# Performance work log

Hardware: AMD Instinct MI355X
Metric: run time of the kernel (lower is better)

## Reference

```python
import jax, jax.numpy as jnp
import numpy as np

S, B, DENC, DD, DE, V, T = 49, 64, 512, 1800, 512, 10000, 20


def setup_inputs() -> dict:
    key = jax.random.key(0)
    ks = jax.random.split(key, 16)
    g = lambda i, shape: jax.random.normal(ks[i], shape, jnp.float32) * 0.02
    z = lambda *shape: jnp.zeros(shape, jnp.float32)
    return {
        "h": jax.random.normal(ks[0], (S, B, DENC), jnp.float32),
        "E": jax.random.randint(ks[1], (T, B), 0, V),
        "emb": g(2, (V, DE)),
        "attn_W1": g(3, (DD, DD + DENC)), "attn_b1": z(DD),
        "attn_w2": g(4, (DD,)), "attn_b2": z(),
        "beta_w": g(5, (DD,)), "beta_b": z(),
        "W_ih": g(6, (4 * DD, DE + DENC)), "W_hh": g(7, (4 * DD, DD)),
        "b_ih": z(4 * DD), "b_hh": z(4 * DD),
        "out_W": g(8, (V, DD + DE + DENC)), "out_b": z(V),
        "ih_W1": g(9, (DD, DENC)), "ih_b1": z(DD), "ih_W2": g(10, (DD, DD)), "ih_b2": z(DD),
        "ic_W1": g(11, (DD, DENC)), "ic_b1": z(DD), "ic_W2": g(12, (DD, DD)), "ic_b2": z(DD),
    }


def _mlp(x, W1, b1, W2, b2):
    return jax.nn.relu(x @ W1.T + b1) @ W2.T + b2


def reference(h, E, emb, attn_W1, attn_b1, attn_w2, attn_b2, beta_w, beta_b,
              W_ih, W_hh, b_ih, b_hh, out_W, out_b,
              ih_W1, ih_b1, ih_W2, ih_b2, ic_W1, ic_b1, ic_W2, ic_b2):
    # h: (S, B, DENC) encoder annotations; E: (T, B) teacher tokens.
    h_avg = h.mean(axis=0)                        # (B, DENC)
    h0 = _mlp(h_avg, ih_W1, ih_b1, ih_W2, ih_b2)  # (B, DD)
    c0 = _mlp(h_avg, ic_W1, ic_b1, ic_W2, ic_b2)  # (B, DD)
    tok0 = jnp.zeros((h.shape[1],), jnp.int32)    # first y_tm1 is token 0

    def step(carry, e_t):
        ht, ct, prev_tok = carry
        # --- additive attention (queries=ht, keys=values=h) ---
        qexp = jnp.broadcast_to(ht[None], h.shape[:2] + (ht.shape[-1],))  # (S,B,DD)
        zpre = jnp.concatenate([qexp, h], axis=-1)                        # (S,B,DD+DENC)
        u = jax.nn.relu(zpre @ attn_W1.T + attn_b1) @ attn_w2 + attn_b2   # (S,B)
        a = jax.nn.softmax(u, axis=0)                                     # softmax over seq
        ctx = jnp.einsum('sb,sbe->be', a, h)                              # (B,DENC)
        beta = jax.nn.sigmoid(ht @ beta_w + beta_b)                       # (B,)
        ctx = ctx * beta[:, None]
        # --- LSTM cell on [embed(E_tm1); context] ---
        x = jnp.concatenate([emb[e_t], ctx], axis=-1)                     # (B,DE+DENC)
        gates = x @ W_ih.T + b_ih + ht @ W_hh.T + b_hh                    # (B,4*DD)
        i_g, f_g, g_g, o_g = jnp.split(gates, 4, axis=-1)
        c_new = jax.nn.sigmoid(f_g) * ct + jax.nn.sigmoid(i_g) * jnp.tanh(g_g)
        h_new = jax.nn.sigmoid(o_g) * jnp.tanh(c_new)
        # --- deep output layer: [h_t; embed(argmax prev logits); ctx] ---
        y_emb = emb[prev_tok]
        logits = jnp.concatenate([h_new, y_emb, ctx], axis=-1) @ out_W.T + out_b
        return (h_new, c_new, jnp.argmax(logits, axis=-1).astype(jnp.int32)), logits

    _, logits = jax.lax.scan(step, (h0, c0, tok0), E[:-1])
    return logits  # (T-1, B, V)
```

## Files before the change

### kernel.cpp

```cpp
#include <hip/hip_runtime.h>
#include <hip/hip_bf16.h>
#include <cmath>


namespace {

constexpr int S = 49, B = 64, DENC = 512, DD = 1800, DE = 512, V = 10000, T = 20;
constexpr int KC = DD + DE + DENC;
constexpr int G4 = 4 * DD;
constexpr int KCP = 2848;
constexpr int DDP = 1824;

typedef __attribute__((ext_vector_type(8))) short short8;
typedef __attribute__((ext_vector_type(4))) float f32x4;

__device__ inline float sigf(float x) { return 1.f / (1.f + expf(-x)); }

__device__ inline ushort f2bf_rne(float x) {
  unsigned u = __float_as_uint(x);
  unsigned r = (u + 0x7FFFu + ((u >> 16) & 1u)) >> 16;
  return (ushort)r;
}
__device__ inline void split1(float x, ushort& h, ushort& l) {
  h = f2bf_rne(x);
  float hf = __uint_as_float(((unsigned)h) << 16);
  l = f2bf_rne(x - hf);
}
__device__ inline void split8(float4 a, float4 b, short8& hi, short8& lo) {
  float v[8] = {a.x, a.y, a.z, a.w, b.x, b.y, b.z, b.w};
#pragma unroll
  for (int i = 0; i < 8; ++i) {
    ushort h, l; split1(v[i], h, l);
    hi[i] = (short)h; lo[i] = (short)l;
  }
}

__global__ __launch_bounds__(256) void hmean_kernel(const float* __restrict__ h,
                                                    float* __restrict__ h_avg) {
  int idx = blockIdx.x * 256 + threadIdx.x;
  if (idx >= B * DENC) return;
  float s = 0.f;
  for (int si = 0; si < S; ++si) s += h[(size_t)si * B * DENC + idx];
  h_avg[idx] = s * (1.0f / (float)S);
}

__global__ __launch_bounds__(256) void mfma_gemm8(
    const ushort* __restrict__ Ahi, const ushort* __restrict__ Alo, int ldap,
    const float* __restrict__ Wa, int ldwa, int Ka,
    const float* __restrict__ Wb, int ldwb, int K,
    float* __restrict__ P, int M, int N, int KP, int kchunk) {
  __shared__ float lds[2][4096];
  const int tid = threadIdx.x;
  const int lane = tid & 63;
  const int wv = tid >> 6;
  const int bn = blockIdx.x * 64;
  const int bm = blockIdx.y * 64;
  const int z = blockIdx.z;
  const int row = lane & 15;
  const int k_begin = z * kchunk;
  const int k_end = min(KP, k_begin + kchunk);
  const int n = bn + wv * 16 + row;

  auto stage = [&](int buf, int k0) {
#pragma unroll
    for (int j = 0; j < 2; ++j) {
      const int r = wv * 2 + j;
      const int lr = r * 8 + (lane >> 3);
      const int pb = lane & 7;
      const int c = pb ^ (lr & 7);
      int col = k0 + c * 4;
      if (col >= K) col = 0;
      int grow = bn + lr;
      if (grow >= N) grow = N - 1;
      const float* src = (col < Ka) ? (Wa + (size_t)grow * ldwa + col)
                                    : (Wb + (size_t)grow * ldwb + (col - Ka));
      __builtin_amdgcn_global_load_lds(
          (const __attribute__((address_space(1))) unsigned int*)src,
          (__attribute__((address_space(3))) unsigned int*)
              &lds[buf][r * 256 + lane * 4],
          16, 0, 0);
    }
    {
      const int lr = wv * 16 + (lane >> 2);
      const int pb = lane & 3;
      const int c = pb ^ (lr & 3);
      const int col = k0 + c * 8;
      const ushort* srcH = Ahi + (size_t)(bm + lr) * ldap + col;
      const ushort* srcL = Alo + (size_t)(bm + lr) * ldap + col;
      __builtin_amdgcn_global_load_lds(
          (const __attribute__((address_space(1))) unsigned int*)srcH,
          (__attribute__((address_space(3))) unsigned int*)
              &lds[buf][2048 + wv * 256 + lane * 4],
          16, 0, 0);
      __builtin_amdgcn_global_load_lds(
          (const __attribute__((address_space(1))) unsigned int*)srcL,
          (__attribute__((address_space(3))) unsigned int*)
              &lds[buf][3072 + wv * 256 + lane * 4],
          16, 0, 0);
    }
  };

  f32x4 acc[4] = {};
  const int nsteps = (k_end > k_begin) ? ((k_end - k_begin) >> 5) : 0;
  if (nsteps) stage(0, k_begin);
  __syncthreads();

  for (int t = 0; t < nsteps; ++t) {
    const int cur = t & 1;
    if (t + 1 < nsteps) stage(cur ^ 1, k_begin + (t + 1) * 32);
    const int lrw = wv * 16 + row;
    const int c0 = (lane >> 4) * 2;
    const float* wbase = &lds[cur][lrw * 32];
    float4 w0 = *(const float4*)(wbase + ((c0 ^ (lrw & 7)) * 4));
    float4 w1 = *(const float4*)(wbase + (((c0 + 1) ^ (lrw & 7)) * 4));
    short8 ah[4], al[4];
#pragma unroll
    for (int ms = 0; ms < 4; ++ms) {
      const int lra = ms * 16 + row;
      const int ca = lane >> 4;
      const int pc = (ca ^ (lra & 3)) * 4;
      ah[ms] = *(const short8*)(&lds[cur][2048 + lra * 16] + pc);
      al[ms] = *(const short8*)(&lds[cur][3072 + lra * 16] + pc);
    }
    short8 wh, wl;
    split8(w0, w1, wh, wl);
#pragma unroll
    for (int ms = 0; ms < 4; ++ms) {
      acc[ms] = __builtin_amdgcn_mfma_f32_16x16x32_bf16(ah[ms], wh, acc[ms], 0, 0, 0);
      acc[ms] = __builtin_amdgcn_mfma_f32_16x16x32_bf16(al[ms], wh, acc[ms], 0, 0, 0);
      acc[ms] = __builtin_amdgcn_mfma_f32_16x16x32_bf16(ah[ms], wl, acc[ms], 0, 0, 0);
    }
    __syncthreads();
  }

  if (n >= N) return;
  float* Pz = P + (size_t)z * ((size_t)M * N);
#pragma unroll
  for (int ms = 0; ms < 4; ++ms) {
    int r0 = bm + ms * 16 + (lane >> 4) * 4;
#pragma unroll
    for (int r = 0; r < 4; ++r)
      Pz[(size_t)(r0 + r) * N + n] = acc[ms][r];
  }
}

template <int ACT>
__global__ __launch_bounds__(256) void reduce_k(const float* __restrict__ P, int nz,
                                                int total4, size_t MN, int N,
                                                const float* __restrict__ bias,
                                                float* __restrict__ C) {
  int i4 = blockIdx.x * 256 + threadIdx.x;
  if (i4 >= total4) return;
  size_t idx = (size_t)i4 * 4;
  float4 s = *(const float4*)(P + idx);
  for (int zz = 1; zz < nz; ++zz) {
    float4 t = *(const float4*)(P + (size_t)zz * MN + idx);
    s.x += t.x; s.y += t.y; s.z += t.z; s.w += t.w;
  }
  if (bias) {
    int nn = (int)(idx % (size_t)N);
    s.x += bias[nn]; s.y += bias[nn + 1]; s.z += bias[nn + 2]; s.w += bias[nn + 3];
  }
  if (ACT == 1) {
    s.x = fmaxf(s.x, 0.f); s.y = fmaxf(s.y, 0.f);
    s.z = fmaxf(s.z, 0.f); s.w = fmaxf(s.w, 0.f);
  }
  *(float4*)(C + idx) = s;
}

__global__ __launch_bounds__(256) void split_row(
    const float* __restrict__ Wa, int ldwa, int Ka,
    int KP, ushort* __restrict__ hi, ushort* __restrict__ lo) {
  const int r = blockIdx.x;
  const float* ra = Wa + (size_t)r * ldwa;
  ushort* hr = hi + (size_t)r * KP;
  ushort* lr = lo + (size_t)r * KP;
  for (int k = threadIdx.x * 4; k < KP; k += 1024) {
    float4 v = {0.f, 0.f, 0.f, 0.f};
    if (k + 4 <= Ka) v = *(const float4*)(ra + k);
    ushort h0, l0, h1, l1, h2, l2, h3, l3;
    split1(v.x, h0, l0); split1(v.y, h1, l1);
    split1(v.z, h2, l2); split1(v.w, h3, l3);
    ushort4 hv = {h0, h1, h2, h3}, lv = {l0, l1, l2, l3};
    *(ushort4*)(hr + k) = hv;
    *(ushort4*)(lr + k) = lv;
  }
}

__global__ __launch_bounds__(256) void attn_u_kernel(const float* __restrict__ Q,
                                                     const float* __restrict__ Hproj,
                                                     const float* __restrict__ w2,
                                                     const float* __restrict__ b2,
                                                     float* __restrict__ u) {
  int s = blockIdx.x, b = blockIdx.y;
  const float4* q4 = (const float4*)(Q + (size_t)b * DD);
  const float4* h4 = (const float4*)(Hproj + ((size_t)s * B + b) * DD);
  const float4* w4 = (const float4*)w2;
  float acc = 0.f;
  for (int i = threadIdx.x; i < DD / 4; i += 256) {
    float4 q = q4[i], hh = h4[i], w = w4[i];
    acc += fmaxf(q.x + hh.x, 0.f) * w.x + fmaxf(q.y + hh.y, 0.f) * w.y +
           fmaxf(q.z + hh.z, 0.f) * w.z + fmaxf(q.w + hh.w, 0.f) * w.w;
  }
  for (int off = 32; off; off >>= 1) acc += __shfl_xor(acc, off);
  __shared__ float red[4];
  if ((threadIdx.x & 63) == 0) red[threadIdx.x >> 6] = acc;
  __syncthreads();
  if (threadIdx.x == 0) u[s * B + b] = red[0] + red[1] + red[2] + red[3] + b2[0];
}

__global__ __launch_bounds__(256) void softmax_ctx_pack(
    const float* __restrict__ u, const float* __restrict__ h,
    const float* __restrict__ ht, const float* __restrict__ beta_w,
    const float* __restrict__ beta_b, const float* __restrict__ emb,
    const int* __restrict__ Et, const int* __restrict__ prev_tok,
    ushort* __restrict__ xcat_hi, ushort* __restrict__ xcat_lo,
    ushort* __restrict__ cat2_hi, ushort* __restrict__ cat2_lo) {
  int b = blockIdx.x, slice = blockIdx.y, tid = threadIdx.x;
  __shared__ float a_sh[S];
  __shared__ float red[4];
  float uv = (tid < S) ? u[tid * B + b] : -INFINITY;
  float m = uv;
  for (int off = 32; off; off >>= 1) m = fmaxf(m, __shfl_xor(m, off));
  if ((tid & 63) == 0) red[tid >> 6] = m;
  __syncthreads();
  m = fmaxf(fmaxf(red[0], red[1]), fmaxf(red[2], red[3]));
  float e = (tid < S) ? expf(uv - m) : 0.f;
  float ssum = e;
  for (int off = 32; off; off >>= 1) ssum += __shfl_xor(ssum, off);
  __syncthreads();
  if ((tid & 63) == 0) red[tid >> 6] = ssum;
  __syncthreads();
  ssum = red[0] + red[1] + red[2] + red[3];
  if (tid < S) a_sh[tid] = e / ssum;
  float acc = 0.f;
  {
    const float4* h4 = (const float4*)(ht + (size_t)b * DD);
    const float4* w4 = (const float4*)beta_w;
    for (int i = tid; i < DD / 4; i += 256) {
      float4 x = h4[i], w = w4[i];
      acc += x.x * w.x + x.y * w.y + x.z * w.z + x.w * w.w;
    }
  }
  for (int off = 32; off; off >>= 1) acc += __shfl_xor(acc, off);
  __syncthreads();
  if ((tid & 63) == 0) red[tid >> 6] = acc;
  __syncthreads();
  float beta = sigf(red[0] + red[1] + red[2] + red[3] + beta_b[0]);

  const size_t xb = (size_t)b * KCP;
  for (int e0 = slice * 128 + tid; e0 < slice * 128 + 128; e0 += 256) {
    float c = 0.f;
    for (int si = 0; si < S; ++si) c += a_sh[si] * h[((size_t)si * B + b) * DENC + e0];
    c *= beta;
    ushort hh, ll; split1(c, hh, ll);
    xcat_hi[xb + DE + e0] = hh;      xcat_lo[xb + DE + e0] = ll;
    cat2_hi[xb + DD + DE + e0] = hh; cat2_lo[xb + DD + DE + e0] = ll;
  }
  int et = Et[b];
  int pt = prev_tok[b];
  for (int e0 = slice * 128 + tid; e0 < slice * 128 + 128; e0 += 256) {
    ushort hh, ll;
    split1(emb[(size_t)et * DE + e0], hh, ll);
    xcat_hi[xb + e0] = hh; xcat_lo[xb + e0] = ll;
    split1(emb[(size_t)pt * DE + e0], hh, ll);
    cat2_hi[xb + DD + e0] = hh; cat2_lo[xb + DD + e0] = ll;
  }
  for (int j = slice * 450 + tid; j < slice * 450 + 450; j += 256) {
    ushort hh, ll; split1(ht[(size_t)b * DD + j], hh, ll);
    xcat_hi[xb + DE + DENC + j] = hh; xcat_lo[xb + DE + DENC + j] = ll;
  }
  if (slice == 3 && tid < KCP - KC) {
    xcat_hi[xb + KC + tid] = 0; xcat_lo[xb + KC + tid] = 0;
    cat2_hi[xb + KC + tid] = 0; cat2_lo[xb + KC + tid] = 0;
  }
}

__global__ __launch_bounds__(256) void lstm_fused(
    const float* __restrict__ P, int nz, const float* __restrict__ b_ih,
    const float* __restrict__ b_hh, float* __restrict__ ct, float* __restrict__ ht,
    ushort* __restrict__ cat2_hi, ushort* __restrict__ cat2_lo,
    ushort* __restrict__ ht_hi, ushort* __restrict__ ht_lo) {
  int idx = blockIdx.x * 256 + threadIdx.x;
  if (idx >= B * DD) return;
  int b = idx / DD, d = idx % DD;
  const size_t MN = (size_t)B * G4;
  float g0 = 0.f, g1 = 0.f, g2 = 0.f, g3 = 0.f;
  for (int zz = 0; zz < nz; ++zz) {
    const float* g = P + (size_t)zz * MN + (size_t)b * G4;
    g0 += g[d]; g1 += g[DD + d]; g2 += g[2 * DD + d]; g3 += g[3 * DD + d];
  }
  g0 += b_ih[d] + b_hh[d];
  g1 += b_ih[DD + d] + b_hh[DD + d];
  g2 += b_ih[2 * DD + d] + b_hh[2 * DD + d];
  g3 += b_ih[3 * DD + d] + b_hh[3 * DD + d];
  float c = sigf(g1) * ct[idx] + sigf(g0) * tanhf(g2);
  float hn = sigf(g3) * tanhf(c);
  ct[idx] = c;
  ht[idx] = hn;
  ushort hh, ll; split1(hn, hh, ll);
  cat2_hi[(size_t)b * KCP + d] = hh; cat2_lo[(size_t)b * KCP + d] = ll;
  ht_hi[(size_t)b * DDP + d] = hh;   ht_lo[(size_t)b * DDP + d] = ll;
  if (d < DDP - DD) {
    ht_hi[(size_t)b * DDP + DD + d] = 0; ht_lo[(size_t)b * DDP + DD + d] = 0;
  }
}

__global__ __launch_bounds__(256) void argmax_kernel(const float* __restrict__ logits,
                                                     int* __restrict__ tok) {
  int b = blockIdx.x;
  const float* row = logits + (size_t)b * V;
  float best = -INFINITY;
  int bi = 0x7fffffff;
  for (int v = threadIdx.x; v < V; v += 256) {
    float x = row[v];
    if (x > best) { best = x; bi = v; }
  }
  for (int off = 32; off; off >>= 1) {
    float ov = __shfl_xor(best, off);
    int oi = __shfl_xor(bi, off);
    if (ov > best || (ov == best && oi < bi)) { best = ov; bi = oi; }
  }
  __shared__ float bv[4];
  __shared__ int bix[4];
  if ((threadIdx.x & 63) == 0) { bv[threadIdx.x >> 6] = best; bix[threadIdx.x >> 6] = bi; }
  __syncthreads();
  if (threadIdx.x == 0) {
    for (int w = 1; w < 4; ++w)
      if (bv[w] > best || (bv[w] == best && bix[w] < bi)) { best = bv[w]; bi = bix[w]; }
    tok[b] = bi;
  }
}

__global__ void zero_tok(int* tok) { if (threadIdx.x < B) tok[threadIdx.x] = 0; }

constexpr size_t OFF_HAVG  = 0;
constexpr size_t OFF_TMP   = OFF_HAVG + 32768;
constexpr size_t OFF_HT    = OFF_TMP + 115200;
constexpr size_t OFF_CT    = OFF_HT + 115200;
constexpr size_t OFF_HPROJ = OFF_CT + 115200;
constexpr size_t OFF_Q     = OFF_HPROJ + 5644800;
constexpr size_t OFF_U     = OFF_Q + 115200;
constexpr size_t OFF_TOK   = OFF_U + 3200;
constexpr size_t OFF_PBUF  = OFF_TOK + 128;
constexpr size_t PBUF_F    = 6400000;
constexpr size_t OFF_USH   = OFF_PBUF + PBUF_F;

constexpr size_t U_HT_HI  = 0;
constexpr size_t U_HT_LO  = U_HT_HI + (size_t)B * DDP;
constexpr size_t U_XC_HI  = U_HT_LO + (size_t)B * DDP;
constexpr size_t U_XC_LO  = U_XC_HI + (size_t)B * KCP;
constexpr size_t U_C2_HI  = U_XC_LO + (size_t)B * KCP;
constexpr size_t U_C2_LO  = U_C2_HI + (size_t)B * KCP;
constexpr size_t U_H_HI   = U_C2_LO + (size_t)B * KCP;
constexpr size_t U_H_LO   = U_H_HI + (size_t)(S * B) * DENC;

}

extern "C" void kernel_launch(void* const* d_in, const int* in_sizes, int n_in,
                              void* d_out, int out_size, void* d_ws, size_t ws_size,
                              hipStream_t stream) {
  const float* h       = (const float*)d_in[0];
  const int*   E       = (const int*)d_in[1];
  const float* emb     = (const float*)d_in[2];
  const float* attn_W1 = (const float*)d_in[3];
  const float* attn_b1 = (const float*)d_in[4];
  const float* attn_w2 = (const float*)d_in[5];
  const float* attn_b2 = (const float*)d_in[6];
  const float* beta_w  = (const float*)d_in[7];
  const float* beta_b  = (const float*)d_in[8];
  const float* W_ih    = (const float*)d_in[9];
  const float* W_hh    = (const float*)d_in[10];
  const float* b_ih    = (const float*)d_in[11];
  const float* b_hh    = (const float*)d_in[12];
  const float* out_W   = (const float*)d_in[13];
  const float* out_b   = (const float*)d_in[14];
  const float* ih_W1   = (const float*)d_in[15];
  const float* ih_b1   = (const float*)d_in[16];
  const float* ih_W2   = (const float*)d_in[17];
  const float* ih_b2   = (const float*)d_in[18];
  const float* ic_W1   = (const float*)d_in[19];
  const float* ic_b1   = (const float*)d_in[20];
  const float* ic_W2   = (const float*)d_in[21];
  const float* ic_b2   = (const float*)d_in[22];

  float* ws    = (float*)d_ws;
  float* havg  = ws + OFF_HAVG;
  float* tmp   = ws + OFF_TMP;
  float* ht    = ws + OFF_HT;
  float* ct    = ws + OFF_CT;
  float* Hproj = ws + OFF_HPROJ;
  float* Q     = ws + OFF_Q;
  float* u     = ws + OFF_U;
  int*   tok   = (int*)(ws + OFF_TOK);
  float* PBUF  = ws + OFF_PBUF;
  ushort* bfb  = (ushort*)(ws + OFF_USH);
  ushort* ht_hi = bfb + U_HT_HI;
  ushort* ht_lo = bfb + U_HT_LO;
  ushort* xc_hi = bfb + U_XC_HI;
  ushort* xc_lo = bfb + U_XC_LO;
  ushort* c2_hi = bfb + U_C2_HI;
  ushort* c2_lo = bfb + U_C2_LO;
  ushort* h_hi  = bfb + U_H_HI;
  ushort* h_lo  = bfb + U_H_LO;
  float* out   = (float*)d_out;

  ushort* hv_hi = xc_hi;
  ushort* hv_lo = xc_lo;
  ushort* t_hi  = c2_hi;
  ushort* t_lo  = c2_lo;

  auto cdiv = [](int a, int b) { return (a + b - 1) / b; };
  const int BIGK = 1 << 28;

  hmean_kernel<<<cdiv(B * DENC, 256), 256, 0, stream>>>(h, havg);
  split_row<<<B, 256, 0, stream>>>(havg, DENC, DENC, DENC, hv_hi, hv_lo);
  mfma_gemm8<<<dim3(cdiv(DD, 64), 1, 4), 256, 0, stream>>>(
      hv_hi, hv_lo, DENC, ih_W1, DENC, BIGK, ih_W1, DENC, DENC,
      PBUF, B, DD, DENC, 128);
  reduce_k<1><<<cdiv(B * DD / 4, 256), 256, 0, stream>>>(
      PBUF, 4, B * DD / 4, (size_t)B * DD, DD, ih_b1, tmp);
  split_row<<<B, 256, 0, stream>>>(tmp, DD, DD, DDP, t_hi, t_lo);
  mfma_gemm8<<<dim3(cdiv(DD, 64), 1, 12), 256, 0, stream>>>(
      t_hi, t_lo, DDP, ih_W2, DD, BIGK, ih_W2, DD, DD,
      PBUF, B, DD, DDP, 160);
  reduce_k<0><<<cdiv(B * DD / 4, 256), 256, 0, stream>>>(
      PBUF, 12, B * DD / 4, (size_t)B * DD, DD, ih_b2, ht);
  mfma_gemm8<<<dim3(cdiv(DD, 64), 1, 4), 256, 0, stream>>>(
      hv_hi, hv_lo, DENC, ic_W1, DENC, BIGK, ic_W1, DENC, DENC,
      PBUF, B, DD, DENC, 128);
  reduce_k<1><<<cdiv(B * DD / 4, 256), 256, 0, stream>>>(
      PBUF, 4, B * DD / 4, (size_t)B * DD, DD, ic_b1, tmp);
  split_row<<<B, 256, 0, stream>>>(tmp, DD, DD, DDP, t_hi, t_lo);
  mfma_gemm8<<<dim3(cdiv(DD, 64), 1, 12), 256, 0, stream>>>(
      t_hi, t_lo, DDP, ic_W2, DD, BIGK, ic_W2, DD, DD,
      PBUF, B, DD, DDP, 160);
  reduce_k<0><<<cdiv(B * DD / 4, 256), 256, 0, stream>>>(
      PBUF, 12, B * DD / 4, (size_t)B * DD, DD, ic_b2, ct);
  split_row<<<B, 256, 0, stream>>>(ht, DD, DD, DDP, ht_hi, ht_lo);
  split_row<<<S * B, 256, 0, stream>>>(h, DENC, DENC, DENC, h_hi, h_lo);
  mfma_gemm8<<<dim3(cdiv(DD, 64), S * B / 64, 1), 256, 0, stream>>>(
      h_hi, h_lo, DENC, attn_W1 + DD, DD + DENC, BIGK, attn_W1 + DD,
      DD + DENC, DENC, Hproj, S * B, DD, DENC, 512);
  reduce_k<0><<<cdiv(S * B * DD / 4, 256), 256, 0, stream>>>(
      Hproj, 1, S * B * DD / 4, (size_t)S * B * DD, DD, attn_b1, Hproj);
  zero_tok<<<1, 64, 0, stream>>>(tok);

  for (int t = 0; t < T - 1; ++t) {
    mfma_gemm8<<<dim3(cdiv(DD, 64), 1, 12), 256, 0, stream>>>(
        ht_hi, ht_lo, DDP, attn_W1, DD + DENC, BIGK, attn_W1, DD + DENC, DD,
        PBUF, B, DD, DDP, 160);
    reduce_k<0><<<cdiv(B * DD / 4, 256), 256, 0, stream>>>(
        PBUF, 12, B * DD / 4, (size_t)B * DD, DD, nullptr, Q);
    attn_u_kernel<<<dim3(S, B), 256, 0, stream>>>(Q, Hproj, attn_w2, attn_b2, u);
    softmax_ctx_pack<<<dim3(B, 4), 256, 0, stream>>>(u, h, ht, beta_w, beta_b, emb,
        E + (size_t)t * B, tok, xc_hi, xc_lo, c2_hi, c2_lo);
    mfma_gemm8<<<dim3(cdiv(G4, 64), 1, 12), 256, 0, stream>>>(
        xc_hi, xc_lo, KCP, W_ih, DE + DENC, DE + DENC, W_hh, DD, KC,
        PBUF, B, G4, KCP, 256);
    lstm_fused<<<cdiv(B * DD, 256), 256, 0, stream>>>(
        PBUF, 12, b_ih, b_hh, ct, ht, c2_hi, c2_lo, ht_hi, ht_lo);
    float* logits_t = out + (size_t)t * B * V;
    mfma_gemm8<<<dim3(cdiv(V, 64), 1, 10), 256, 0, stream>>>(
        c2_hi, c2_lo, KCP, out_W, KC, BIGK, out_W, KC, KC,
        PBUF, B, V, KCP, 288);
    reduce_k<0><<<cdiv(B * V / 4, 256), 256, 0, stream>>>(
        PBUF, 10, B * V / 4, (size_t)B * V, V, out_b, logits_t);
    argmax_kernel<<<B, 256, 0, stream>>>(logits_t, tok);
  }
  (void)in_sizes; (void)n_in; (void)out_size; (void)ws_size;
}
```

Baseline: 2.374 ms.

## Triple-buffer GEMM staging with vmcnt waits and fuse argmax into logits reduce

The GEMM kernel moves from double to triple-buffered LDS staging. It prefetches two k-steps ahead and replaces __syncthreads with explicit vmcnt waits plus raw s_barrier, so global-to-LDS loads overlap compute for longer. The logits split-K reduction now also computes the per-row argmax with a packed 64-bit key and atomicMax, which removes the separate argmax kernel and its reread of the logits. The cost is more LDS per block, which may lower occupancy, plus reliance on hand-placed waitcnt correctness and atomics reset inside lstm_fused.

```diff
diff --git a/kernel.cpp b/kernel.cpp
--- a/kernel.cpp
+++ b/kernel.cpp
@@ -33,6 +33,10 @@
     ushort h, l; split1(v[i], h, l);
     hi[i] = (short)h; lo[i] = (short)l;
   }
+}
+__device__ inline unsigned fkey(float f) {
+  unsigned u = __float_as_uint(f);
+  return (u & 0x80000000u) ? ~u : (u | 0x80000000u);
 }
 
 __global__ __launch_bounds__(256) void hmean_kernel(const float* __restrict__ h,
@@ -44,12 +48,12 @@
   h_avg[idx] = s * (1.0f / (float)S);
 }
 
-__global__ __launch_bounds__(256) void mfma_gemm8(
+__global__ __launch_bounds__(256) void mfma_gemm10(
     const ushort* __restrict__ Ahi, const ushort* __restrict__ Alo, int ldap,
     const float* __restrict__ Wa, int ldwa, int Ka,
     const float* __restrict__ Wb, int ldwb, int K,
     float* __restrict__ P, int M, int N, int KP, int kchunk) {
-  __shared__ float lds[2][4096];
+  __shared__ float lds[3][4096];
   const int tid = threadIdx.x;
   const int lane = tid & 63;
   const int wv = tid >> 6;
@@ -102,12 +106,18 @@
 
   f32x4 acc[4] = {};
   const int nsteps = (k_end > k_begin) ? ((k_end - k_begin) >> 5) : 0;
-  if (nsteps) stage(0, k_begin);
-  __syncthreads();
-
+  if (nsteps > 0) stage(0, k_begin);
+  if (nsteps > 1) stage(1, k_begin + 32);
+  __builtin_amdgcn_sched_barrier(0);
+  if (nsteps > 1) asm volatile("s_waitcnt vmcnt(4)" ::: "memory");
+  else            asm volatile("s_waitcnt vmcnt(0)" ::: "memory");
+  __builtin_amdgcn_s_barrier();
+  __builtin_amdgcn_sched_barrier(0);
+
+  int cur = 0;
   for (int t = 0; t < nsteps; ++t) {
-    const int cur = t & 1;
-    if (t + 1 < nsteps) stage(cur ^ 1, k_begin + (t + 1) * 32);
+    const int nx2 = (cur >= 1) ? (cur - 1) : (cur + 2);
+    if (t + 2 < nsteps) stage(nx2, k_begin + (t + 2) * 32);
     const int lrw = wv * 16 + row;
     const int c0 = (lane >> 4) * 2;
     const float* wbase = &lds[cur][lrw * 32];
@@ -130,7 +140,12 @@
       acc[ms] = __builtin_amdgcn_mfma_f32_16x16x32_bf16(al[ms], wh, acc[ms], 0, 0, 0);
       acc[ms] = __builtin_amdgcn_mfma_f32_16x16x32_bf16(ah[ms], wl, acc[ms], 0, 0, 0);
     }
-    __syncthreads();
+    __builtin_amdgcn_sched_barrier(0);
+    if (t + 2 < nsteps) asm volatile("s_waitcnt vmcnt(4)" ::: "memory");
+    else                asm volatile("s_waitcnt vmcnt(0)" ::: "memory");
+    __builtin_amdgcn_s_barrier();
+    __builtin_amdgcn_sched_barrier(0);
+    cur = (cur >= 2) ? 0 : (cur + 1);
   }
 
   if (n >= N) return;
@@ -166,6 +181,46 @@
     s.z = fmaxf(s.z, 0.f); s.w = fmaxf(s.w, 0.f);
   }
   *(float4*)(C + idx) = s;
+}
+
+__global__ __launch_bounds__(256) void reduce_lg(const float* __restrict__ P, int nz,
+                                                 const float* __restrict__ bias,
+                                                 float* __restrict__ C,
+                                                 unsigned long long* __restrict__ amax) {
+  const int seg = blockIdx.x, b = blockIdx.y;
+  const int tid = threadIdx.x;
+  const size_t MN = (size_t)B * V;
+  unsigned long long best = 0;
+  for (int i = tid; i < 250; i += 256) {
+    const int n = seg * 1000 + i * 4;
+    const size_t idx = (size_t)b * V + n;
+    float4 s = *(const float4*)(P + idx);
+    for (int zz = 1; zz < nz; ++zz) {
+      float4 t = *(const float4*)(P + (size_t)zz * MN + idx);
+      s.x += t.x; s.y += t.y; s.z += t.z; s.w += t.w;
+    }
+    s.x += bias[n]; s.y += bias[n + 1]; s.z += bias[n + 2]; s.w += bias[n + 3];
+    *(float4*)(C + idx) = s;
+    float v[4] = {s.x, s.y, s.z, s.w};
+#pragma unroll
+    for (int j = 0; j < 4; ++j) {
+      unsigned long long k =
+          ((unsigned long long)fkey(v[j]) << 32) | (unsigned)(~(n + j));
+      if (k > best) best = k;
+    }
+  }
+  for (int off = 32; off; off >>= 1) {
+    unsigned long long o = __shfl_xor(best, off);
+    if (o > best) best = o;
+  }
+  __shared__ unsigned long long red[4];
+  if ((tid & 63) == 0) red[tid >> 6] = best;
+  __syncthreads();
+  if (tid == 0) {
+    for (int w = 1; w < 4; ++w)
+      if (red[w] > best) best = red[w];
+    atomicMax(&amax[b], best);
+  }
 }
 
 __global__ __launch_bounds__(256) void split_row(
@@ -213,7 +268,7 @@
     const float* __restrict__ u, const float* __restrict__ h,
     const float* __restrict__ ht, const float* __restrict__ beta_w,
     const float* __restrict__ beta_b, const float* __restrict__ emb,
-    const int* __restrict__ Et, const int* __restrict__ prev_tok,
+    const int* __restrict__ Et, const unsigned long long* __restrict__ amax,
     ushort* __restrict__ xcat_hi, ushort* __restrict__ xcat_lo,
     ushort* __restrict__ cat2_hi, ushort* __restrict__ cat2_lo) {
   int b = blockIdx.x, slice = blockIdx.y, tid = threadIdx.x;
@@ -258,7 +313,7 @@
     cat2_hi[xb + DD + DE + e0] = hh; cat2_lo[xb + DD + DE + e0] = ll;
   }
   int et = Et[b];
-  int pt = prev_tok[b];
+  int pt = (int)(~(unsigned)(amax[b] & 0xFFFFFFFFull));
   for (int e0 = slice * 128 + tid; e0 < slice * 128 + 128; e0 += 256) {
     ushort hh, ll;
     split1(emb[(size_t)et * DE + e0], hh, ll);
@@ -280,8 +335,10 @@
     const float* __restrict__ P, int nz, const float* __restrict__ b_ih,
     const float* __restrict__ b_hh, float* __restrict__ ct, float* __restrict__ ht,
     ushort* __restrict__ cat2_hi, ushort* __restrict__ cat2_lo,
-    ushort* __restrict__ ht_hi, ushort* __restrict__ ht_lo) {
+    ushort* __restrict__ ht_hi, ushort* __restrict__ ht_lo,
+    unsigned long long* __restrict__ amax) {
   int idx = blockIdx.x * 256 + threadIdx.x;
+  if (idx < B) amax[idx] = 0ull;
   if (idx >= B * DD) return;
   int b = idx / DD, d = idx % DD;
   const size_t MN = (size_t)B * G4;
@@ -306,33 +363,9 @@
   }
 }
 
-__global__ __launch_bounds__(256) void argmax_kernel(const float* __restrict__ logits,
-                                                     int* __restrict__ tok) {
-  int b = blockIdx.x;
-  const float* row = logits + (size_t)b * V;
-  float best = -INFINITY;
-  int bi = 0x7fffffff;
-  for (int v = threadIdx.x; v < V; v += 256) {
-    float x = row[v];
-    if (x > best) { best = x; bi = v; }
-  }
-  for (int off = 32; off; off >>= 1) {
-    float ov = __shfl_xor(best, off);
-    int oi = __shfl_xor(bi, off);
-    if (ov > best || (ov == best && oi < bi)) { best = ov; bi = oi; }
-  }
-  __shared__ float bv[4];
-  __shared__ int bix[4];
-  if ((threadIdx.x & 63) == 0) { bv[threadIdx.x >> 6] = best; bix[threadIdx.x >> 6] = bi; }
-  __syncthreads();
-  if (threadIdx.x == 0) {
-    for (int w = 1; w < 4; ++w)
-      if (bv[w] > best || (bv[w] == best && bix[w] < bi)) { best = bv[w]; bi = bix[w]; }
-    tok[b] = bi;
-  }
-}
-
-__global__ void zero_tok(int* tok) { if (threadIdx.x < B) tok[threadIdx.x] = 0; }
+__global__ void init_amax(unsigned long long* amax) {
+  if (threadIdx.x < B) amax[threadIdx.x] = 0x00000000FFFFFFFFull;
+}
 
 constexpr size_t OFF_HAVG  = 0;
 constexpr size_t OFF_TMP   = OFF_HAVG + 32768;
@@ -392,7 +425,7 @@
   float* Hproj = ws + OFF_HPROJ;
   float* Q     = ws + OFF_Q;
   float* u     = ws + OFF_U;
-  int*   tok   = (int*)(ws + OFF_TOK);
+  unsigned long long* amax = (unsigned long long*)(ws + OFF_TOK);
   float* PBUF  = ws + OFF_PBUF;
   ushort* bfb  = (ushort*)(ws + OFF_USH);
   ushort* ht_hi = bfb + U_HT_HI;
@@ -415,58 +448,56 @@
 
   hmean_kernel<<<cdiv(B * DENC, 256), 256, 0, stream>>>(h, havg);
   split_row<<<B, 256, 0, stream>>>(havg, DENC, DENC, DENC, hv_hi, hv_lo);
-  mfma_gemm8<<<dim3(cdiv(DD, 64), 1, 4), 256, 0, stream>>>(
+  mfma_gemm10<<<dim3(cdiv(DD, 64), 1, 4), 256, 0, stream>>>(
       hv_hi, hv_lo, DENC, ih_W1, DENC, BIGK, ih_W1, DENC, DENC,
       PBUF, B, DD, DENC, 128);
   reduce_k<1><<<cdiv(B * DD / 4, 256), 256, 0, stream>>>(
       PBUF, 4, B * DD / 4, (size_t)B * DD, DD, ih_b1, tmp);
   split_row<<<B, 256, 0, stream>>>(tmp, DD, DD, DDP, t_hi, t_lo);
-  mfma_gemm8<<<dim3(cdiv(DD, 64), 1, 12), 256, 0, stream>>>(
+  mfma_gemm10<<<dim3(cdiv(DD, 64), 1, 12), 256, 0, stream>>>(
       t_hi, t_lo, DDP, ih_W2, DD, BIGK, ih_W2, DD, DD,
       PBUF, B, DD, DDP, 160);
   reduce_k<0><<<cdiv(B * DD / 4, 256), 256, 0, stream>>>(
       PBUF, 12, B * DD / 4, (size_t)B * DD, DD, ih_b2, ht);
-  mfma_gemm8<<<dim3(cdiv(DD, 64), 1, 4), 256, 0, stream>>>(
+  mfma_gemm10<<<dim3(cdiv(DD, 64), 1, 4), 256, 0, stream>>>(
       hv_hi, hv_lo, DENC, ic_W1, DENC, BIGK, ic_W1, DENC, DENC,
       PBUF, B, DD, DENC, 128);
   reduce_k<1><<<cdiv(B * DD / 4, 256), 256, 0, stream>>>(
       PBUF, 4, B * DD / 4, (size_t)B * DD, DD, ic_b1, tmp);
   split_row<<<B, 256, 0, stream>>>(tmp, DD, DD, DDP, t_hi, t_lo);
-  mfma_gemm8<<<dim3(cdiv(DD, 64), 1, 12), 256, 0, stream>>>(
+  mfma_gemm10<<<dim3(cdiv(DD, 64), 1, 12), 256, 0, stream>>>(
       t_hi, t_lo, DDP, ic_W2, DD, BIGK, ic_W2, DD, DD,
       PBUF, B, DD, DDP, 160);
   reduce_k<0><<<cdiv(B * DD / 4, 256), 256, 0, stream>>>(
       PBUF, 12, B * DD / 4, (size_t)B * DD, DD, ic_b2, ct);
   split_row<<<B, 256, 0, stream>>>(ht, DD, DD, DDP, ht_hi, ht_lo);
   split_row<<<S * B, 256, 0, stream>>>(h, DENC, DENC, DENC, h_hi, h_lo);
-  mfma_gemm8<<<dim3(cdiv(DD, 64), S * B / 64, 1), 256, 0, stream>>>(
+  mfma_gemm10<<<dim3(cdiv(DD, 64), S * B / 64, 1), 256, 0, stream>>>(
       h_hi, h_lo, DENC, attn_W1 + DD, DD + DENC, BIGK, attn_W1 + DD,
       DD + DENC, DENC, Hproj, S * B, DD, DENC, 512);
   reduce_k<0><<<cdiv(S * B * DD / 4, 256), 256, 0, stream>>>(
       Hproj, 1, S * B * DD / 4, (size_t)S * B * DD, DD, attn_b1, Hproj);
-  zero_tok<<<1, 64, 0, stream>>>(tok);
+  init_amax<<<1, 64, 0, stream>>>(amax);
 
   for (int t = 0; t < T - 1; ++t) {
-    mfma_gemm8<<<dim3(cdiv(DD, 64), 1, 12), 256, 0, stream>>>(
+    mfma_gemm10<<<dim3(cdiv(DD, 64), 1, 12), 256, 0, stream>>>(
         ht_hi, ht_lo, DDP, attn_W1, DD + DENC, BIGK, attn_W1, DD + DENC, DD,
         PBUF, B, DD, DDP, 160);
     reduce_k<0><<<cdiv(B * DD / 4, 256), 256, 0, stream>>>(
         PBUF, 12, B * DD / 4, (size_t)B * DD, DD, nullptr, Q);
     attn_u_kernel<<<dim3(S, B), 256, 0, stream>>>(Q, Hproj, attn_w2, attn_b2, u);
     softmax_ctx_pack<<<dim3(B, 4), 256, 0, stream>>>(u, h, ht, beta_w, beta_b, emb,
-        E + (size_t)t * B, tok, xc_hi, xc_lo, c2_hi, c2_lo);
-    mfma_gemm8<<<dim3(cdiv(G4, 64), 1, 12), 256, 0, stream>>>(
+        E + (size_t)t * B, amax, xc_hi, xc_lo, c2_hi, c2_lo);
+    mfma_gemm10<<<dim3(cdiv(G4, 64), 1, 12), 256, 0, stream>>>(
         xc_hi, xc_lo, KCP, W_ih, DE + DENC, DE + DENC, W_hh, DD, KC,
         PBUF, B, G4, KCP, 256);
     lstm_fused<<<cdiv(B * DD, 256), 256, 0, stream>>>(
-        PBUF, 12, b_ih, b_hh, ct, ht, c2_hi, c2_lo, ht_hi, ht_lo);
+        PBUF, 12, b_ih, b_hh, ct, ht, c2_hi, c2_lo, ht_hi, ht_lo, amax);
     float* logits_t = out + (size_t)t * B * V;
-    mfma_gemm8<<<dim3(cdiv(V, 64), 1, 10), 256, 0, stream>>>(
+    mfma_gemm10<<<dim3(cdiv(V, 64), 1, 10), 256, 0, stream>>>(
         c2_hi, c2_lo, KCP, out_W, KC, BIGK, out_W, KC, KC,
         PBUF, B, V, KCP, 288);
-    reduce_k<0><<<cdiv(B * V / 4, 256), 256, 0, stream>>>(
-        PBUF, 10, B * V / 4, (size_t)B * V, V, out_b, logits_t);
-    argmax_kernel<<<B, 256, 0, stream>>>(logits_t, tok);
+    reduce_lg<<<dim3(10, B), 256, 0, stream>>>(PBUF, 10, out_b, logits_t, amax);
   }
   (void)in_sizes; (void)n_in; (void)out_size; (void)ws_size;
 }
```

Result: faster. 2.145 ms (-9.7%).
